# Kernel optimization log

Hardware: AMD Instinct MI355X
Metric: run time of the kernel (lower is better)

The kernel has to match this reference:

```python
import jax, jax.numpy as jnp
import numpy as np

D_MODEL = 2048
N_HEADS = 16
N_KV = 4
D_K = D_MODEL // N_HEADS  # 128
B, T = 2, 2048


def setup_inputs() -> dict:
    key = jax.random.key(0)
    ks = jax.random.split(key, 10)
    s = 1.0 / np.sqrt(D_MODEL)
    x = jax.random.normal(ks[0], (B, T, D_MODEL), dtype=jnp.float32)
    mask = jnp.ones((B, 1, T, T), dtype=bool)
    Wq = jax.random.uniform(ks[1], (D_MODEL, D_MODEL), minval=-s, maxval=s, dtype=jnp.float32)
    bq = jax.random.uniform(ks[2], (D_MODEL,), minval=-s, maxval=s, dtype=jnp.float32)
    Wk = jax.random.uniform(ks[3], (D_MODEL, N_KV * D_K), minval=-s, maxval=s, dtype=jnp.float32)
    bk = jax.random.uniform(ks[4], (N_KV * D_K,), minval=-s, maxval=s, dtype=jnp.float32)
    Wv = jax.random.uniform(ks[5], (D_MODEL, N_KV * D_K), minval=-s, maxval=s, dtype=jnp.float32)
    bv = jax.random.uniform(ks[6], (N_KV * D_K,), minval=-s, maxval=s, dtype=jnp.float32)
    Wo = jax.random.uniform(ks[7], (D_MODEL, D_MODEL), minval=-s, maxval=s, dtype=jnp.float32)
    bo = jax.random.uniform(ks[8], (D_MODEL,), minval=-s, maxval=s, dtype=jnp.float32)
    return {"x": x, "mask": mask, "Wq": Wq, "bq": bq, "Wk": Wk, "bk": bk,
            "Wv": Wv, "bv": bv, "Wo": Wo, "bo": bo}


def reference(x, mask, Wq, bq, Wk, bk, Wv, bv, Wo, bo):
    Bn, Tn, _ = x.shape
    g = N_HEADS // N_KV
    # projections
    q = (x @ Wq + bq).reshape(Bn, Tn, N_HEADS, D_K).transpose(0, 2, 1, 3)  # [B,H,T,d]
    k = (x @ Wk + bk).reshape(Bn, Tn, N_KV, D_K).transpose(0, 2, 1, 3)     # [B,Hk,T,d]
    v = (x @ Wv + bv).reshape(Bn, Tn, N_KV, D_K).transpose(0, 2, 1, 3)
    # GQA broadcast: group Q heads as [B,Hk,g,T,d]; no repeat_interleave copy
    qg = q.reshape(Bn, N_KV, g, Tn, D_K)
    scores = jnp.einsum('bkgqd,bkld->bkgql', qg, k) / jnp.sqrt(jnp.float32(D_K))
    scores = jnp.where(mask[:, :, None, :, :], scores, jnp.float32(-1e9))
    attn = jax.nn.softmax(scores, axis=-1)  # dropout=0 (eval)
    out = jnp.einsum('bkgql,bkld->bkgqd', attn, v)  # [B,Hk,g,T,d]
    out = out.reshape(Bn, N_HEADS, Tn, D_K).transpose(0, 2, 1, 3).reshape(Bn, Tn, D_MODEL)
    return out @ Wo + bo
```

## Files before the change

kernel.cpp:

```cpp
#include <hip/hip_runtime.h>

typedef __attribute__((ext_vector_type(8))) short short8;
typedef __attribute__((ext_vector_type(4))) short short4v;
typedef __attribute__((ext_vector_type(4))) float f32x4;

__device__ __forceinline__ unsigned short f2bf(float f) {
  union { float f; unsigned u; } v; v.f = f;
  unsigned u = v.u;
  return (unsigned short)((u + 0x7fffu + ((u >> 16) & 1u)) >> 16);
}

__device__ __forceinline__ void gload16(void* lds, const void* g) {
  __builtin_amdgcn_global_load_lds(
      (__attribute__((address_space(1))) unsigned int*)g,
      (__attribute__((address_space(3))) unsigned int*)lds, 16, 0, 0);
}

__global__ void cast_f32_bf16(const float* __restrict__ in,
                              unsigned short* __restrict__ out, int n8) {
  int i = blockIdx.x * 256 + threadIdx.x;
  if (i >= n8) return;
  const float4* p = (const float4*)in + (size_t)i * 2;
  float4 a = p[0], b = p[1];
  union { unsigned short u[8]; short8 v; } o;
  o.u[0] = f2bf(a.x); o.u[1] = f2bf(a.y); o.u[2] = f2bf(a.z); o.u[3] = f2bf(a.w);
  o.u[4] = f2bf(b.x); o.u[5] = f2bf(b.y); o.u[6] = f2bf(b.z); o.u[7] = f2bf(b.w);
  *(short8*)(out + (size_t)i * 8) = o.v;
}

__global__ void trans_cast(const float* __restrict__ src,
                           unsigned short* __restrict__ dst,
                           int N, int rowOff) {
  __shared__ float tile[32][33];
  int n0 = blockIdx.x * 32, k0 = blockIdx.y * 32;
  int c = threadIdx.x & 31, rr = threadIdx.x >> 5;
#pragma unroll
  for (int p = 0; p < 4; ++p) {
    int r = p * 8 + rr;
    tile[r][c] = src[(size_t)(k0 + r) * N + n0 + c];
  }
  __syncthreads();
#pragma unroll
  for (int p = 0; p < 4; ++p) {
    int r = p * 8 + rr;
    dst[(size_t)(rowOff + n0 + r) * 2048 + k0 + c] = f2bf(tile[c][r]);
  }
}

__global__ __launch_bounds__(256) void gemm_bf16(
    const unsigned short* __restrict__ A, const unsigned short* __restrict__ Bt,
    int K, int mode,
    const float* __restrict__ b0, const float* __restrict__ b1,
    const float* __restrict__ b2,
    unsigned short* __restrict__ oq, unsigned short* __restrict__ ok,
    unsigned short* __restrict__ ov, float* __restrict__ of) {
  __shared__ unsigned short lds[16384];
  int tid = threadIdx.x, w = tid >> 6, lane = tid & 63, lo = lane & 15, hi = lane >> 4;
  int wr = w >> 1, wc = w & 1;
  int m0 = blockIdx.x * 128, n0 = blockIdx.y * 128;
  f32x4 acc[4][4] = {};
  const char* Ab = (const char*)A;
  const char* Bb = (const char*)Bt;
  char* L = (char*)lds;

  for (int k0 = 0; k0 < K; k0 += 64) {
#pragma unroll
    for (int j = 0; j < 4; ++j) {
      int o = j * 4096 + w * 1024 + lane * 16;
      int r = o >> 7;
      int cb = (o & 127) ^ ((r & 7) << 4);
      gload16(L + j * 4096 + w * 1024,
              Ab + (size_t)(m0 + r) * K * 2 + k0 * 2 + cb);
    }
#pragma unroll
    for (int j = 0; j < 4; ++j) {
      int o = j * 4096 + w * 1024 + lane * 16;
      int r = o >> 7;
      int cb = (o & 127) ^ ((r & 7) << 4);
      gload16(L + 16384 + j * 4096 + w * 1024,
              Bb + (size_t)(n0 + r) * K * 2 + k0 * 2 + cb);
    }
    __syncthreads();
    short8 af[2][4], bf[2][4];
#pragma unroll
    for (int ks = 0; ks < 2; ++ks) {
#pragma unroll
      for (int i = 0; i < 4; ++i) {
        int row = wr * 64 + i * 16 + lo;
        af[ks][i] = *(const short8*)(L + ((row * 128 + ks * 64 + hi * 16) ^ ((row & 7) << 4)));
      }
#pragma unroll
      for (int j = 0; j < 4; ++j) {
        int row = wc * 64 + j * 16 + lo;
        bf[ks][j] = *(const short8*)(L + 16384 + ((row * 128 + ks * 64 + hi * 16) ^ ((row & 7) << 4)));
      }
    }
#pragma unroll
    for (int ks = 0; ks < 2; ++ks)
#pragma unroll
      for (int i = 0; i < 4; ++i)
#pragma unroll
        for (int j = 0; j < 4; ++j)
          acc[i][j] = __builtin_amdgcn_mfma_f32_16x16x32_bf16(af[ks][i], bf[ks][j], acc[i][j], 0, 0, 0);
    __syncthreads();
  }

#pragma unroll
  for (int i = 0; i < 4; ++i) {
    int mbase = m0 + wr * 64 + i * 16 + hi * 4;
#pragma unroll
    for (int j = 0; j < 4; ++j) {
      int n = n0 + wc * 64 + j * 16 + lo;
      if (mode == 0) {
        float bias;
        if (n < 2048) bias = b0[n];
        else if (n < 2560) bias = b1[n - 2048];
        else bias = b2[n - 2560];
#pragma unroll
        for (int r = 0; r < 4; ++r) {
          int mm = mbase + r;
          int b = mm >> 11, t = mm & 2047;
          float val = acc[i][j][r] + bias;
          if (n < 2048) {
            int h = n >> 7, d = n & 127;
            oq[(((size_t)(b * 16 + h)) * 2048 + t) * 128 + d] =
                f2bf(val * (0.08838834764831845f * 1.4426950408889634f));
          } else if (n < 2560) {
            int kvh = (n - 2048) >> 7, d = (n - 2048) & 127;
            ok[(((size_t)(b * 4 + kvh)) * 2048 + t) * 128 + d] = f2bf(val);
          } else {
            int kvh = (n - 2560) >> 7, d = (n - 2560) & 127;
            ov[(((size_t)(b * 4 + kvh)) * 128 + d) * 2048 + t] = f2bf(val);
          }
        }
      } else {
        float bias = b0[n];
#pragma unroll
        for (int r = 0; r < 4; ++r)
          of[(size_t)(mbase + r) * 2048 + n] = acc[i][j][r] + bias;
      }
    }
  }
}

__device__ __forceinline__ void stageK(char* KLb, const char* kcb, int w, int lane, int t0) {
#pragma unroll
  for (int j = 0; j < 4; ++j) {
    int o = j * 4096 + w * 1024 + lane * 16;
    int row = o >> 8;
    gload16(KLb + j * 4096 + w * 1024, kcb + t0 * 256 + (o ^ ((row & 7) << 4)));
  }
}
__device__ __forceinline__ void stageV(char* VLb, const char* vcb, int w, int lane, int t0) {
#pragma unroll
  for (int j = 0; j < 4; ++j) {
    int o = j * 4096 + w * 1024 + lane * 16;
    int d = o >> 7, low = o & 127;
    gload16(VLb + j * 4096 + w * 1024,
            vcb + (size_t)d * 4096 + t0 * 2 + (low ^ ((d & 7) << 4)));
  }
}

__global__ __launch_bounds__(256, 2) void attn_fwd(
    const unsigned short* __restrict__ q, const unsigned short* __restrict__ kg,
    const unsigned short* __restrict__ vtg, unsigned short* __restrict__ attn) {
  __shared__ unsigned short kbuf[16384];
  __shared__ unsigned short vbuf[16384];
  __shared__ unsigned short pbuf[8192];
  int tid = threadIdx.x, w = tid >> 6, lane = tid & 63, lo = lane & 15, hi = lane >> 4;
  int tq0 = blockIdx.x * 128, h = blockIdx.y, b = blockIdx.z, kvh = h >> 2;
  int qrow = tq0 + w * 32;

  const unsigned short* qbase = q + ((size_t)(b * 16 + h)) * 2048 * 128;
  short8 qf[2][4];
#pragma unroll
  for (int j2 = 0; j2 < 2; ++j2)
#pragma unroll
    for (int ks = 0; ks < 4; ++ks)
      qf[j2][ks] = *(const short8*)(qbase + (size_t)(qrow + j2 * 16 + lo) * 128 + ks * 32 + hi * 8);

  f32x4 oacc[2][8] = {};
  float mrow[2] = {-1e30f, -1e30f}, lsum[2] = {0.f, 0.f};

  const char* kcb = (const char*)(kg + ((size_t)(b * 4 + kvh)) * 2048 * 128);
  const char* vcb = (const char*)(vtg + ((size_t)(b * 4 + kvh)) * 128 * 2048);
  char* KL = (char*)kbuf;
  char* VL = (char*)vbuf;
  char* PL = (char*)pbuf + w * 4096;

  stageK(KL, kcb, w, lane, 0);
  stageV(VL, vcb, w, lane, 0);
  __syncthreads();
  int buf = 0;

  for (int t0 = 0; t0 < 2048; t0 += 64) {
    if (t0 + 64 < 2048) {
      stageK(KL + (buf ^ 1) * 16384, kcb, w, lane, t0 + 64);
      stageV(VL + (buf ^ 1) * 16384, vcb, w, lane, t0 + 64);
    }
    const char* KB = KL + buf * 16384;
    const char* VB = VL + buf * 16384;

    f32x4 s[4][2] = {};
    __builtin_amdgcn_s_setprio(1);
#pragma unroll
    for (int f = 0; f < 4; ++f) {
      int row = f * 16 + lo;
      int sw = (row & 7) << 4;
#pragma unroll
      for (int ks = 0; ks < 4; ++ks) {
        short8 kf = *(const short8*)(KB + ((row * 256 + ks * 64 + hi * 16) ^ sw));
#pragma unroll
        for (int j2 = 0; j2 < 2; ++j2)
          s[f][j2] = __builtin_amdgcn_mfma_f32_16x16x32_bf16(kf, qf[j2][ks], s[f][j2], 0, 0, 0);
      }
    }
    __builtin_amdgcn_s_setprio(0);

    float a[2];
#pragma unroll
    for (int j2 = 0; j2 < 2; ++j2) {
      float a0 = fmaxf(fmaxf(s[0][j2][0], s[0][j2][1]), fmaxf(s[0][j2][2], s[0][j2][3]));
      float a1 = fmaxf(fmaxf(s[1][j2][0], s[1][j2][1]), fmaxf(s[1][j2][2], s[1][j2][3]));
      float a2 = fmaxf(fmaxf(s[2][j2][0], s[2][j2][1]), fmaxf(s[2][j2][2], s[2][j2][3]));
      float a3 = fmaxf(fmaxf(s[3][j2][0], s[3][j2][1]), fmaxf(s[3][j2][2], s[3][j2][3]));
      a[j2] = fmaxf(fmaxf(a0, a1), fmaxf(a2, a3));
    }
    int okv = (a[0] <= mrow[0] + 8.f) && (a[1] <= mrow[1] + 8.f);
    if (!__all(okv)) {
      float fs[2];
#pragma unroll
      for (int j2 = 0; j2 < 2; ++j2) {
        float am = a[j2];
        am = fmaxf(am, __shfl_xor(am, 16));
        am = fmaxf(am, __shfl_xor(am, 32));
        float mnew = fmaxf(mrow[j2], am);
        fs[j2] = __builtin_amdgcn_exp2f(mrow[j2] - mnew);
        mrow[j2] = mnew;
        lsum[j2] *= fs[j2];
      }
#pragma unroll
      for (int i = 0; i < 2; ++i)
#pragma unroll
        for (int r = 0; r < 4; ++r) {
          float fsr = __shfl(fs[i], hi * 4 + r);
#pragma unroll
          for (int nf = 0; nf < 8; ++nf) oacc[i][nf][r] *= fsr;
        }
    }

#pragma unroll
    for (int j2 = 0; j2 < 2; ++j2) {
      int qq = j2 * 16 + lo;
      int sw = (qq & 7) << 4;
      float m = mrow[j2];
      float acc = 0.f;
#pragma unroll
      for (int f = 0; f < 4; ++f) {
        float p0 = __builtin_amdgcn_exp2f(s[f][j2][0] - m);
        float p1 = __builtin_amdgcn_exp2f(s[f][j2][1] - m);
        float p2 = __builtin_amdgcn_exp2f(s[f][j2][2] - m);
        float p3 = __builtin_amdgcn_exp2f(s[f][j2][3] - m);
        union { unsigned short u[4]; short4v v; } pk;
        pk.u[0] = f2bf(p0); pk.u[1] = f2bf(p1); pk.u[2] = f2bf(p2); pk.u[3] = f2bf(p3);
        *(short4v*)(PL + ((qq * 128 + f * 32 + hi * 8) ^ sw)) = pk.v;
        acc += (p0 + p1) + (p2 + p3);
      }
      lsum[j2] += acc;
    }
    __threadfence_block();

    short8 pfr[2][2];
#pragma unroll
    for (int i = 0; i < 2; ++i) {
      int qq = i * 16 + lo;
      int sw = (qq & 7) << 4;
#pragma unroll
      for (int ks2 = 0; ks2 < 2; ++ks2)
        pfr[i][ks2] = *(const short8*)(PL + ((qq * 128 + ks2 * 64 + hi * 16) ^ sw));
    }
    __builtin_amdgcn_s_setprio(1);
#pragma unroll
    for (int nf = 0; nf < 8; ++nf) {
      int d = nf * 16 + lo;
      int sw = (d & 7) << 4;
#pragma unroll
      for (int ks2 = 0; ks2 < 2; ++ks2) {
        short8 vf = *(const short8*)(VB + ((d * 128 + ks2 * 64 + hi * 16) ^ sw));
#pragma unroll
        for (int i = 0; i < 2; ++i)
          oacc[i][nf] = __builtin_amdgcn_mfma_f32_16x16x32_bf16(pfr[i][ks2], vf, oacc[i][nf], 0, 0, 0);
      }
    }
    __builtin_amdgcn_s_setprio(0);
    __syncthreads();
    buf ^= 1;
  }

  unsigned short* ob = attn + ((size_t)b * 2048) * 2048 + h * 128;
#pragma unroll
  for (int i = 0; i < 2; ++i) {
    float ls = lsum[i];
    ls += __shfl_xor(ls, 16);
    ls += __shfl_xor(ls, 32);
    float linv = 1.0f / ls;
#pragma unroll
    for (int r = 0; r < 4; ++r) {
      float lr = __shfl(linv, hi * 4 + r);
      int t = qrow + i * 16 + hi * 4 + r;
#pragma unroll
      for (int nf = 0; nf < 8; ++nf)
        ob[(size_t)t * 2048 + nf * 16 + lo] = f2bf(oacc[i][nf][r] * lr);
    }
  }
}

extern "C" void kernel_launch(void* const* d_in, const int* in_sizes, int n_in,
                              void* d_out, int out_size, void* d_ws, size_t ws_size,
                              hipStream_t stream) {
  const float* x  = (const float*)d_in[0];
  const float* Wq = (const float*)d_in[2];
  const float* bq = (const float*)d_in[3];
  const float* Wk = (const float*)d_in[4];
  const float* bk = (const float*)d_in[5];
  const float* Wv = (const float*)d_in[6];
  const float* bv = (const float*)d_in[7];
  const float* Wo = (const float*)d_in[8];
  const float* bo = (const float*)d_in[9];
  float* out = (float*)d_out;

  char* ws = (char*)d_ws;
  unsigned short* xb    = (unsigned short*)(ws);
  unsigned short* wqkvT = (unsigned short*)(ws + 16777216);
  unsigned short* woT   = (unsigned short*)(ws + 29360128);
  unsigned short* qb    = (unsigned short*)(ws + 37748736);
  unsigned short* kbw   = (unsigned short*)(ws + 54525952);
  unsigned short* vtw   = (unsigned short*)(ws + 58720256);
  unsigned short* attnb = (unsigned short*)(ws + 62914560);

  cast_f32_bf16<<<dim3(4096), dim3(256), 0, stream>>>(x, xb, 1048576);
  trans_cast<<<dim3(64, 64), dim3(256), 0, stream>>>(Wq, wqkvT, 2048, 0);
  trans_cast<<<dim3(16, 64), dim3(256), 0, stream>>>(Wk, wqkvT, 512, 2048);
  trans_cast<<<dim3(16, 64), dim3(256), 0, stream>>>(Wv, wqkvT, 512, 2560);
  trans_cast<<<dim3(64, 64), dim3(256), 0, stream>>>(Wo, woT, 2048, 0);

  gemm_bf16<<<dim3(32, 24), dim3(256), 0, stream>>>(
      xb, wqkvT, 2048, 0, bq, bk, bv, qb, kbw, vtw, nullptr);

  attn_fwd<<<dim3(16, 16, 2), dim3(256), 0, stream>>>(qb, kbw, vtw, attnb);

  gemm_bf16<<<dim3(32, 16), dim3(256), 0, stream>>>(
      attnb, woT, 2048, 1, bo, nullptr, nullptr, nullptr, nullptr, nullptr, out);
}
```

Baseline: 243.7 us.

## Switch attention to 32x32x16 MFMA and pass P via permlane32 swap

```diff
diff --git a/kernel.cpp b/kernel.cpp
--- a/kernel.cpp
+++ b/kernel.cpp
@@ -1,13 +1,22 @@
 #include <hip/hip_runtime.h>
+#include <hip/hip_bf16.h>
 
 typedef __attribute__((ext_vector_type(8))) short short8;
 typedef __attribute__((ext_vector_type(4))) short short4v;
 typedef __attribute__((ext_vector_type(4))) float f32x4;
+typedef __attribute__((ext_vector_type(16))) float f32x16;
+typedef __attribute__((ext_vector_type(2))) unsigned uint2v;
 
 __device__ __forceinline__ unsigned short f2bf(float f) {
   union { float f; unsigned u; } v; v.f = f;
   unsigned u = v.u;
   return (unsigned short)((u + 0x7fffu + ((u >> 16) & 1u)) >> 16);
+}
+
+__device__ __forceinline__ unsigned packbf2(float a, float b) {
+  union { __hip_bfloat162 h; unsigned u; } c;
+  c.h = __float22bfloat162_rn(float2{a, b});
+  return c.u;
 }
 
 __device__ __forceinline__ void gload16(void* lds, const void* g) {
@@ -147,17 +156,18 @@
 #pragma unroll
   for (int j = 0; j < 4; ++j) {
     int o = j * 4096 + w * 1024 + lane * 16;
-    int row = o >> 8;
-    gload16(KLb + j * 4096 + w * 1024, kcb + t0 * 256 + (o ^ ((row & 7) << 4)));
+    int row = o >> 8, col = o & 255;
+    gload16(KLb + j * 4096 + w * 1024,
+            kcb + (size_t)(t0 + row) * 256 + (col ^ ((row & 15) << 4)));
   }
 }
 __device__ __forceinline__ void stageV(char* VLb, const char* vcb, int w, int lane, int t0) {
 #pragma unroll
   for (int j = 0; j < 4; ++j) {
     int o = j * 4096 + w * 1024 + lane * 16;
-    int d = o >> 7, low = o & 127;
+    int d = o >> 7, col = o & 127;
     gload16(VLb + j * 4096 + w * 1024,
-            vcb + (size_t)d * 4096 + t0 * 2 + (low ^ ((d & 7) << 4)));
+            vcb + (size_t)d * 4096 + t0 * 2 + (col ^ ((d & 7) << 4)));
   }
 }
 
@@ -166,27 +176,24 @@
     const unsigned short* __restrict__ vtg, unsigned short* __restrict__ attn) {
   __shared__ unsigned short kbuf[16384];
   __shared__ unsigned short vbuf[16384];
-  __shared__ unsigned short pbuf[8192];
-  int tid = threadIdx.x, w = tid >> 6, lane = tid & 63, lo = lane & 15, hi = lane >> 4;
+  int tid = threadIdx.x, w = tid >> 6, lane = tid & 63;
+  int l31 = lane & 31, hi5 = lane >> 5;
   int tq0 = blockIdx.x * 128, h = blockIdx.y, b = blockIdx.z, kvh = h >> 2;
   int qrow = tq0 + w * 32;
 
   const unsigned short* qbase = q + ((size_t)(b * 16 + h)) * 2048 * 128;
-  short8 qf[2][4];
-#pragma unroll
-  for (int j2 = 0; j2 < 2; ++j2)
-#pragma unroll
-    for (int ks = 0; ks < 4; ++ks)
-      qf[j2][ks] = *(const short8*)(qbase + (size_t)(qrow + j2 * 16 + lo) * 128 + ks * 32 + hi * 8);
-
-  f32x4 oacc[2][8] = {};
-  float mrow[2] = {-1e30f, -1e30f}, lsum[2] = {0.f, 0.f};
+  short8 qf[8];
+#pragma unroll
+  for (int ds_ = 0; ds_ < 8; ++ds_)
+    qf[ds_] = *(const short8*)(qbase + (size_t)(qrow + l31) * 128 + ds_ * 16 + hi5 * 8);
+
+  f32x16 oacc[4] = {};
+  float mrow = -1e30f, lsum = 0.f;
 
   const char* kcb = (const char*)(kg + ((size_t)(b * 4 + kvh)) * 2048 * 128);
   const char* vcb = (const char*)(vtg + ((size_t)(b * 4 + kvh)) * 128 * 2048);
   char* KL = (char*)kbuf;
   char* VL = (char*)vbuf;
-  char* PL = (char*)pbuf + w * 4096;
 
   stageK(KL, kcb, w, lane, 0);
   stageV(VL, vcb, w, lane, 0);
@@ -201,95 +208,78 @@
     const char* KB = KL + buf * 16384;
     const char* VB = VL + buf * 16384;
 
-    f32x4 s[4][2] = {};
+    f32x16 s[2] = {};
     __builtin_amdgcn_s_setprio(1);
 #pragma unroll
-    for (int f = 0; f < 4; ++f) {
-      int row = f * 16 + lo;
-      int sw = (row & 7) << 4;
-#pragma unroll
-      for (int ks = 0; ks < 4; ++ks) {
-        short8 kf = *(const short8*)(KB + ((row * 256 + ks * 64 + hi * 16) ^ sw));
-#pragma unroll
-        for (int j2 = 0; j2 < 2; ++j2)
-          s[f][j2] = __builtin_amdgcn_mfma_f32_16x16x32_bf16(kf, qf[j2][ks], s[f][j2], 0, 0, 0);
+    for (int ds_ = 0; ds_ < 8; ++ds_) {
+#pragma unroll
+      for (int f = 0; f < 2; ++f) {
+        int row = f * 32 + l31;
+        short8 kf = *(const short8*)(KB + ((row * 256 + ds_ * 32 + hi5 * 16) ^ ((row & 15) << 4)));
+        s[f] = __builtin_amdgcn_mfma_f32_32x32x16_bf16(kf, qf[ds_], s[f], 0, 0, 0);
       }
     }
     __builtin_amdgcn_s_setprio(0);
 
-    float a[2];
-#pragma unroll
-    for (int j2 = 0; j2 < 2; ++j2) {
-      float a0 = fmaxf(fmaxf(s[0][j2][0], s[0][j2][1]), fmaxf(s[0][j2][2], s[0][j2][3]));
-      float a1 = fmaxf(fmaxf(s[1][j2][0], s[1][j2][1]), fmaxf(s[1][j2][2], s[1][j2][3]));
-      float a2 = fmaxf(fmaxf(s[2][j2][0], s[2][j2][1]), fmaxf(s[2][j2][2], s[2][j2][3]));
-      float a3 = fmaxf(fmaxf(s[3][j2][0], s[3][j2][1]), fmaxf(s[3][j2][2], s[3][j2][3]));
-      a[j2] = fmaxf(fmaxf(a0, a1), fmaxf(a2, a3));
-    }
-    int okv = (a[0] <= mrow[0] + 8.f) && (a[1] <= mrow[1] + 8.f);
-    if (!__all(okv)) {
-      float fs[2];
-#pragma unroll
-      for (int j2 = 0; j2 < 2; ++j2) {
-        float am = a[j2];
-        am = fmaxf(am, __shfl_xor(am, 16));
-        am = fmaxf(am, __shfl_xor(am, 32));
-        float mnew = fmaxf(mrow[j2], am);
-        fs[j2] = __builtin_amdgcn_exp2f(mrow[j2] - mnew);
-        mrow[j2] = mnew;
-        lsum[j2] *= fs[j2];
-      }
-#pragma unroll
-      for (int i = 0; i < 2; ++i)
+    float am = fmaxf(s[0][0], s[0][1]);
+#pragma unroll
+    for (int r = 2; r < 16; ++r) am = fmaxf(am, s[0][r]);
+#pragma unroll
+    for (int r = 0; r < 16; ++r) am = fmaxf(am, s[1][r]);
+
+    if (!__all(am <= mrow + 8.f)) {
+      float ar = fmaxf(am, __shfl_xor(am, 32));
+      float mnew = fmaxf(mrow, ar);
+      float fsv = __builtin_amdgcn_exp2f(mrow - mnew);
+      mrow = mnew;
+      lsum *= fsv;
+#pragma unroll
+      for (int g = 0; g < 4; ++g)
 #pragma unroll
         for (int r = 0; r < 4; ++r) {
-          float fsr = __shfl(fs[i], hi * 4 + r);
-#pragma unroll
-          for (int nf = 0; nf < 8; ++nf) oacc[i][nf][r] *= fsr;
+          float fsr = __shfl(fsv, r + 8 * g + 4 * hi5);
+#pragma unroll
+          for (int db = 0; db < 4; ++db) oacc[db][4 * g + r] *= fsr;
         }
     }
 
-#pragma unroll
-    for (int j2 = 0; j2 < 2; ++j2) {
-      int qq = j2 * 16 + lo;
-      int sw = (qq & 7) << 4;
-      float m = mrow[j2];
-      float acc = 0.f;
-#pragma unroll
-      for (int f = 0; f < 4; ++f) {
-        float p0 = __builtin_amdgcn_exp2f(s[f][j2][0] - m);
-        float p1 = __builtin_amdgcn_exp2f(s[f][j2][1] - m);
-        float p2 = __builtin_amdgcn_exp2f(s[f][j2][2] - m);
-        float p3 = __builtin_amdgcn_exp2f(s[f][j2][3] - m);
-        union { unsigned short u[4]; short4v v; } pk;
-        pk.u[0] = f2bf(p0); pk.u[1] = f2bf(p1); pk.u[2] = f2bf(p2); pk.u[3] = f2bf(p3);
-        *(short4v*)(PL + ((qq * 128 + f * 32 + hi * 8) ^ sw)) = pk.v;
-        acc += (p0 + p1) + (p2 + p3);
-      }
-      lsum[j2] += acc;
-    }
-    __threadfence_block();
-
-    short8 pfr[2][2];
-#pragma unroll
-    for (int i = 0; i < 2; ++i) {
-      int qq = i * 16 + lo;
-      int sw = (qq & 7) << 4;
-#pragma unroll
-      for (int ks2 = 0; ks2 < 2; ++ks2)
-        pfr[i][ks2] = *(const short8*)(PL + ((qq * 128 + ks2 * 64 + hi * 16) ^ sw));
-    }
+    unsigned pk01[2][4], pk23[2][4];
+    float accl = 0.f;
+#pragma unroll
+    for (int f = 0; f < 2; ++f)
+#pragma unroll
+      for (int g = 0; g < 4; ++g) {
+        float p0 = __builtin_amdgcn_exp2f(s[f][4 * g + 0] - mrow);
+        float p1 = __builtin_amdgcn_exp2f(s[f][4 * g + 1] - mrow);
+        float p2 = __builtin_amdgcn_exp2f(s[f][4 * g + 2] - mrow);
+        float p3 = __builtin_amdgcn_exp2f(s[f][4 * g + 3] - mrow);
+        pk01[f][g] = packbf2(p0, p1);
+        pk23[f][g] = packbf2(p2, p3);
+        accl += (p0 + p1) + (p2 + p3);
+      }
+    lsum += accl;
+
+    short8 pA[4];
+#pragma unroll
+    for (int f = 0; f < 2; ++f)
+#pragma unroll
+      for (int p = 0; p < 2; ++p) {
+        uint2v a01 = __builtin_amdgcn_permlane32_swap(pk01[f][2 * p], pk01[f][2 * p + 1], false, false);
+        uint2v a23 = __builtin_amdgcn_permlane32_swap(pk23[f][2 * p], pk23[f][2 * p + 1], false, false);
+        union { unsigned u[4]; short8 v; } pa;
+        pa.u[0] = a01.x; pa.u[1] = a23.x; pa.u[2] = a01.y; pa.u[3] = a23.y;
+        pA[2 * f + p] = pa.v;
+      }
+
     __builtin_amdgcn_s_setprio(1);
 #pragma unroll
-    for (int nf = 0; nf < 8; ++nf) {
-      int d = nf * 16 + lo;
+    for (int db = 0; db < 4; ++db) {
+      int d = db * 32 + l31;
       int sw = (d & 7) << 4;
 #pragma unroll
-      for (int ks2 = 0; ks2 < 2; ++ks2) {
-        short8 vf = *(const short8*)(VB + ((d * 128 + ks2 * 64 + hi * 16) ^ sw));
-#pragma unroll
-        for (int i = 0; i < 2; ++i)
-          oacc[i][nf] = __builtin_amdgcn_mfma_f32_16x16x32_bf16(pfr[i][ks2], vf, oacc[i][nf], 0, 0, 0);
+      for (int step = 0; step < 4; ++step) {
+        short8 vf = *(const short8*)(VB + ((d * 128 + step * 32 + hi5 * 16) ^ sw));
+        oacc[db] = __builtin_amdgcn_mfma_f32_32x32x16_bf16(pA[step], vf, oacc[db], 0, 0, 0);
       }
     }
     __builtin_amdgcn_s_setprio(0);
@@ -298,21 +288,18 @@
   }
 
   unsigned short* ob = attn + ((size_t)b * 2048) * 2048 + h * 128;
-#pragma unroll
-  for (int i = 0; i < 2; ++i) {
-    float ls = lsum[i];
-    ls += __shfl_xor(ls, 16);
-    ls += __shfl_xor(ls, 32);
-    float linv = 1.0f / ls;
+  float ls = lsum + __shfl_xor(lsum, 32);
+  float linv = 1.0f / ls;
+#pragma unroll
+  for (int g = 0; g < 4; ++g)
 #pragma unroll
     for (int r = 0; r < 4; ++r) {
-      float lr = __shfl(linv, hi * 4 + r);
-      int t = qrow + i * 16 + hi * 4 + r;
-#pragma unroll
-      for (int nf = 0; nf < 8; ++nf)
-        ob[(size_t)t * 2048 + nf * 16 + lo] = f2bf(oacc[i][nf][r] * lr);
-    }
-  }
+      float lr = __shfl(linv, r + 8 * g + 4 * hi5);
+      int t = qrow + r + 8 * g + 4 * hi5;
+#pragma unroll
+      for (int db = 0; db < 4; ++db)
+        ob[(size_t)t * 2048 + db * 32 + l31] = f2bf(oacc[db][4 * g + r] * lr);
+    }
 }
 
 extern "C" void kernel_launch(void* const* d_in, const int* in_sizes, int n_in,
```

Result: no change. 241.6 us (-0.9%).
